# Optimization experiments

Measured on AMD Instinct MI355X. Metric: run time of the kernel, lower is better.

## Reference

```python
import jax, jax.numpy as jnp
import numpy as np
from jax import lax

LB, UB = 0.0, 0.1
N_ITERS = 32  # fixed-point iterations for water-filling rebalance


def _conv(x, w, b):
    y = lax.conv_general_dilated(x, w, (1, 1), ((1, 1), (1, 1)),
                                 dimension_numbers=("NCHW", "OIHW", "NCHW"))
    return y + b[None, :, None, None]


def _maxpool2(x):
    return lax.reduce_window(x, -jnp.inf, lax.max, (1, 1, 2, 2), (1, 1, 2, 2), "VALID")


def _linear(x, w, b):
    return x @ w.T + b


def _gru(x_num, W_ih, W_hh, b_ih, b_hh):
    # x_num: [B, S, N]; torch GRU gate order r, z, n
    B = x_num.shape[0]
    H = W_hh.shape[1]
    xs = jnp.swapaxes(x_num, 0, 1)  # [S, B, N]

    def step(h, x_t):
        gi = x_t @ W_ih.T + b_ih            # [B, 3H]
        gh = h @ W_hh.T + b_hh              # [B, 3H]
        i_r, i_z, i_n = jnp.split(gi, 3, axis=-1)
        h_r, h_z, h_n = jnp.split(gh, 3, axis=-1)
        r = jax.nn.sigmoid(i_r + h_r)
        z = jax.nn.sigmoid(i_z + h_z)
        n = jnp.tanh(i_n + r * h_n)
        h_new = (1.0 - z) * n + z * h
        return h_new, None

    h0 = jnp.zeros((B, H), dtype=x_num.dtype)
    h_last, _ = lax.scan(step, h0, xs)
    return h_last


def _rebalance_one(w):
    # vectorized fixed-point version of the per-sample while-loop water-filling
    def body(carry, _):
        old, wc = carry
        leftover = jnp.sum(old - wc)
        mask = wc != UB
        s = jnp.sum(jnp.where(mask, wc, 0.0))
        gift = jnp.where(mask & (s > 0), leftover * wc / jnp.where(s > 0, s, 1.0), 0.0)
        new_old = wc + gift
        new_wc = jnp.clip(new_old, LB, UB)
        return (new_old, new_wc), None

    init = (w, jnp.clip(w, LB, UB))
    (_, wc), _ = lax.scan(body, init, None, length=N_ITERS)
    return wc


def setup_inputs() -> dict:
    key = jax.random.key(0)
    ks = jax.random.split(key, 16)
    B, S, N, H_IMG, W_IMG, HID = 16, 60, 50, 64, 60, 128
    fc_in = 64 * (H_IMG // 4) * (W_IMG // 4)  # 15360
    sc = 0.05
    return {
        "x_num": jax.random.normal(ks[0], (B, S, N), jnp.float32),
        "x_img": jax.random.uniform(ks[1], (B, N, H_IMG, W_IMG), jnp.float32),
        "conv1_w": jax.random.normal(ks[2], (32, 1, 3, 3), jnp.float32) * sc,
        "conv1_b": jnp.zeros((32,), jnp.float32),
        "conv2_w": jax.random.normal(ks[3], (64, 32, 3, 3), jnp.float32) * sc,
        "conv2_b": jnp.zeros((64,), jnp.float32),
        "fc1_w": jax.random.normal(ks[4], (64, fc_in), jnp.float32) * 0.01,
        "fc1_b": jnp.zeros((64,), jnp.float32),
        "fc_binary_w": jax.random.normal(ks[5], (1, 64), jnp.float32) * sc,
        "fc_binary_b": jnp.zeros((1,), jnp.float32),
        "fc2_w": jax.random.normal(ks[6], (128, 64), jnp.float32) * sc,
        "fc2_b": jnp.zeros((128,), jnp.float32),
        "W_ih": jax.random.normal(ks[7], (3 * HID, N), jnp.float32) * sc,
        "W_hh": jax.random.normal(ks[8], (3 * HID, HID), jnp.float32) * sc,
        "b_ih": jnp.zeros((3 * HID,), jnp.float32),
        "b_hh": jnp.zeros((3 * HID,), jnp.float32),
        "gru_fc_w": jax.random.normal(ks[9], (N, HID), jnp.float32) * sc,
        "gru_fc_b": jnp.zeros((N,), jnp.float32),
        "fusion_w": jax.random.normal(ks[10], (64, N + 128), jnp.float32) * sc,
        "fusion_b": jnp.zeros((64,), jnp.float32),
        "final_w": jax.random.normal(ks[11], (N, 64), jnp.float32) * sc,
        "final_b": jnp.zeros((N,), jnp.float32),
    }


def reference(x_num, x_img, conv1_w, conv1_b, conv2_w, conv2_b, fc1_w, fc1_b,
              fc_binary_w, fc_binary_b, fc2_w, fc2_b, W_ih, W_hh, b_ih, b_hh,
              gru_fc_w, gru_fc_b, fusion_w, fusion_b, final_w, final_b):
    B, S, N = x_num.shape
    # GRU branch: last hidden -> Linear -> [B, N]
    h_last = _gru(x_num, W_ih, W_hh, b_ih, b_hh)
    numerical_features = _linear(h_last, gru_fc_w, gru_fc_b)

    # CNN branch on per-stock chart images
    xi = x_img.reshape(B * N, 1, x_img.shape[2], x_img.shape[3])
    h = _maxpool2(jax.nn.relu(_conv(xi, conv1_w, conv1_b)))
    h = _maxpool2(jax.nn.relu(_conv(h, conv2_w, conv2_b)))
    h = h.reshape(B * N, -1)
    feats = jax.nn.relu(_linear(h, fc1_w, fc1_b))
    binary_pred = jax.nn.sigmoid(_linear(feats, fc_binary_w, fc_binary_b))
    cnn_features = _linear(feats, fc2_w, fc2_b).reshape(B, N, -1).mean(axis=1)

    fused = jax.nn.relu(_linear(jnp.concatenate([numerical_features, cnn_features], axis=1), fusion_w, fusion_b))
    w = jax.nn.softmax(_linear(fused, final_w, final_b), axis=1)
    portfolio_weights = jax.vmap(_rebalance_one)(w)
    return portfolio_weights, binary_pred.reshape(B, N)
```

## Files before the change

kernel.cpp:

```cpp
#include <hip/hip_runtime.h>
#include <hip/hip_bf16.h>
#include <hip/hip_fp16.h>

typedef unsigned short ushort_t;
typedef short short8_t __attribute__((ext_vector_type(8)));
typedef _Float16 half8_t __attribute__((ext_vector_type(8)));
typedef _Float16 h2 __attribute__((ext_vector_type(2)));
typedef float f32x4 __attribute__((ext_vector_type(4)));
typedef float f32x16 __attribute__((ext_vector_type(16)));

#define NBATCH 16
#define SEQ    60
#define NSTK   50
#define HID    128
#define G3     384
#define NIMG   800
#define IH     64
#define IW     60
#define P1H    32
#define P1W    30
#define P2C    64
#define FCIN   15360

#define OFF_WHHF   0u
#define OFF_WPREP  24576u
#define OFF_WFC1   33792u
#define OFF_GI     525312u
#define OFF_HLAST  893952u
#define OFF_POOL2  896000u
#define OFF_FC2O   7040000u
#define OFF_PART   7142400u
#define OFF_W1H    7961600u
#define WS_FLOATS  7961760u

#define E_WHH  49152
#define E_WPR  18432
#define E_FC1  983040
#define E_W1H  160
#define E_TOT  (E_WHH + E_WPR + E_FC1 + E_W1H)

struct __align__(16) ConvS {
    ushort_t pool1t[18][4][32][8];
    union {
        float    imgp[35][60];
        ushort_t pool2s[64][120];
    } u;
};
struct __align__(16) GruS {
    ushort_t hb[2][16 * 136];
};
#define SMEM_BYTES 52224

__device__ __forceinline__ float fast_sig(float x) {
    const float e = __expf(-x);
    return __builtin_amdgcn_rcpf(1.f + e);
}
__device__ __forceinline__ float fast_tanh(float x) {
    const float xc = fmaxf(fminf(x, 15.f), -15.f);
    const float e = __expf(2.f * xc);
    return (e - 1.f) * __builtin_amdgcn_rcpf(e + 1.f);
}
__device__ __forceinline__ h2 hmax2v(h2 a, h2 b) {
    h2 r;
    r[0] = a[0] > b[0] ? a[0] : b[0];
    r[1] = a[1] > b[1] ? a[1] : b[1];
    return r;
}

__global__ __launch_bounds__(384) void k_pre(const float* __restrict__ xnum,
                                             const float* __restrict__ wih,
                                             const float* __restrict__ bih,
                                             const float* __restrict__ whh,
                                             const float* __restrict__ c2w,
                                             const float* __restrict__ fc1w,
                                             const float* __restrict__ c1w,
                                             const float* __restrict__ c1b,
                                             float* __restrict__ GI,
                                             ushort_t* __restrict__ whhf,
                                             ushort_t* __restrict__ wprep,
                                             ushort_t* __restrict__ wfc1,
                                             unsigned int* __restrict__ w1h)
{
    const int bid = blockIdx.x;
    if (bid < 960) {
        const int s = bid >> 4, b = bid & 15;
        const int j = threadIdx.x;
        const float* xr = xnum + (size_t)(b * SEQ + s) * NSTK;
        const float* wr = wih + (size_t)j * NSTK;
        float a = bih[j];
        #pragma unroll 10
        for (int k = 0; k < NSTK; ++k) a = fmaf(xr[k], wr[k], a);
        GI[((size_t)s * 16 + b) * G3 + j] = a;
        return;
    }
    const int idx = (bid - 960) * 384 + threadIdx.x;
    if (idx < E_WHH) {
        const int e = idx;
        const int i = e & 7, l = (e >> 3) & 63, ksj = e >> 9;
        const int ks = ksj & 3, jt = ksj >> 2;
        const int j = jt * 16 + (l & 15);
        const int k = ks * 32 + ((l >> 4) << 3) + i;
        __hip_bfloat16 hv = __float2bfloat16(whh[j * HID + k]);
        whhf[e] = *(ushort_t*)&hv;
    } else if (idx < E_WHH + E_WPR) {
        const int e = idx - E_WHH;
        const int i = e & 7, l = (e >> 3) & 63, rest = e >> 9;
        const int ks = rest & 1, mt = rest >> 1;
        const int tap = mt % 9, mm = mt / 9;
        const int oc = mm * 32 + (l & 31);
        const int ic = ks * 16 + ((l >> 5) << 3) + i;
        const _Float16 hv = (_Float16)c2w[((size_t)oc * 32 + ic) * 9 + tap];
        wprep[e] = *(const ushort_t*)&hv;
    } else if (idx < E_WHH + E_WPR + E_FC1) {
        const int e = idx - (E_WHH + E_WPR);
        const int i = e & 7, l = (e >> 3) & 63, rest = e >> 9;
        const int n = rest & 3, T = rest >> 2;
        const int oc = n * 16 + (l & 15);
        const int k = T * 32 + ((l >> 4) << 3) + i;
        __hip_bfloat16 hv = __float2bfloat16(fc1w[(size_t)oc * FCIN + k]);
        wfc1[e] = *(ushort_t*)&hv;
    } else if (idx < E_TOT) {
        const int e = idx - (E_WHH + E_WPR + E_FC1);
        if (e < 144) {
            const int p = e / 9, tap = e - p * 9;
            const int ch0 = (p >> 2) * 8 + (p & 3) * 2;
            const _Float16 lo = (_Float16)c1w[ch0 * 9 + tap];
            const _Float16 hi = (_Float16)c1w[(ch0 + 1) * 9 + tap];
            w1h[p * 9 + tap] = ((unsigned)*(const ushort_t*)&hi << 16) | *(const ushort_t*)&lo;
        } else {
            const int p = e - 144;
            const int ch0 = (p >> 2) * 8 + (p & 3) * 2;
            const _Float16 lo = (_Float16)c1b[ch0];
            const _Float16 hi = (_Float16)c1b[ch0 + 1];
            w1h[144 + p] = ((unsigned)*(const ushort_t*)&hi << 16) | *(const ushort_t*)&lo;
        }
    }
}

__global__ __launch_bounds__(512, 2) void k_mega(const float* __restrict__ x_img,
                                                 const unsigned int* __restrict__ w1h,
                                                 const float* __restrict__ c2b,
                                                 const ushort_t* __restrict__ wprep,
                                                 const float* __restrict__ GI,
                                                 const ushort_t* __restrict__ whhf,
                                                 const float* __restrict__ bhh,
                                                 ushort_t* __restrict__ pool2,
                                                 float* __restrict__ hlast)
{
    extern __shared__ char smraw[];
    const int tid = threadIdx.x;
    const int bid = blockIdx.x;

    if (bid == 0) {
        GruS* g = (GruS*)smraw;
        const int w = tid >> 6, l = tid & 63;
        const int arow = l & 15, kq = l >> 4;
        const int hh = w * 16 + (l & 15);
        const int b0 = (l >> 4) * 4;
        short8_t wfr[3][4];
        #pragma unroll
        for (int g3 = 0; g3 < 3; ++g3)
            #pragma unroll
            for (int ks = 0; ks < 4; ++ks)
                wfr[g3][ks] = *(const short8_t*)&whhf[((((g3 * 8 + w) * 4 + ks) * 64 + l) * 8)];
        const float bhr = bhh[hh];
        const float bhz = bhh[128 + hh];
        const float bhn = bhh[256 + hh];
        float h[4] = {0.f, 0.f, 0.f, 0.f};
        for (int i = tid; i < 1088; i += 512) ((unsigned int*)g->hb[0])[i] = 0u;
        __syncthreads();

        int cur = 0;
        for (int s = 0; s < SEQ; ++s) {
            const float* gis = GI + ((size_t)s * 16 + b0) * G3 + hh;
            float cr[4], cz[4], cn[4];
            #pragma unroll
            for (int r = 0; r < 4; ++r) {
                cr[r] = gis[r * G3];
                cz[r] = gis[r * G3 + 128];
                cn[r] = gis[r * G3 + 256];
            }
            f32x4 ar = {0.f, 0.f, 0.f, 0.f};
            f32x4 az = {0.f, 0.f, 0.f, 0.f};
            f32x4 an = {0.f, 0.f, 0.f, 0.f};
            #pragma unroll
            for (int ks = 0; ks < 4; ++ks) {
                const short8_t af = *(const short8_t*)&g->hb[cur][arow * 136 + ks * 32 + kq * 8];
                ar = __builtin_amdgcn_mfma_f32_16x16x32_bf16(af, wfr[0][ks], ar, 0, 0, 0);
                az = __builtin_amdgcn_mfma_f32_16x16x32_bf16(af, wfr[1][ks], az, 0, 0, 0);
                an = __builtin_amdgcn_mfma_f32_16x16x32_bf16(af, wfr[2][ks], an, 0, 0, 0);
            }
            const int nxt = cur ^ 1;
            #pragma unroll
            for (int r = 0; r < 4; ++r) {
                const float rg = fast_sig(cr[r] + ar[r] + bhr);
                const float zg = fast_sig(cz[r] + az[r] + bhz);
                const float ng = fast_tanh(cn[r] + rg * (an[r] + bhn));
                h[r] = (1.f - zg) * ng + zg * h[r];
                __hip_bfloat16 t = __float2bfloat16(h[r]);
                g->hb[nxt][(b0 + r) * 136 + hh] = *(ushort_t*)&t;
            }
            __syncthreads();
            cur = nxt;
        }
        #pragma unroll
        for (int r = 0; r < 4; ++r) hlast[(b0 + r) * HID + hh] = h[r];
        return;
    }

    ConvS* c = (ConvS*)smraw;
    const int img  = (bid - 1) >> 1;
    const int half = (bid - 1) & 1;
    const float* xim = x_img + (size_t)img * (IH * IW);
    const int rowbase = 29 * half;

    {
        const short8_t z = {0, 0, 0, 0, 0, 0, 0, 0};
        const int zrow = half ? 17 : 0;
        if (tid < 128) {
            const int cg = tid >> 5, xs = tid & 31;
            *(short8_t*)&c->pool1t[zrow][cg][xs][0] = z;
        } else if (tid < 272) {
            const int q = tid - 128;
            const int ly = q / 8, cg = (q >> 1) & 3, xs = (q & 1) * 31;
            *(short8_t*)&c->pool1t[ly][cg][xs][0] = z;
        }
    }
    {
        const f32x4* src = (const f32x4*)(xim + rowbase * IW);
        f32x4* dst = (f32x4*)c->u.imgp;
        for (int i = tid; i < 525; i += 512) dst[i] = src[i];
    }
    __syncthreads();

    if (tid < 510) {
        const int gj = tid / 30, px = tid - gj * 30;
        const int g = half * 15 + gj;
        const int ly = gj + 1 - half;
        const h2 z2 = {(_Float16)0.f, (_Float16)0.f};
        h2 patch2[4][4];
        #pragma unroll
        for (int yy = 0; yy < 4; ++yy) {
            const int giy = 2 * g - 1 + yy;
            const int liy = giy - rowbase;
            #pragma unroll
            for (int xx = 0; xx < 4; ++xx) {
                const int ix = 2 * px - 1 + xx;
                const float v = (giy >= 0 && giy < IH && ix >= 0 && ix < IW)
                                    ? c->u.imgp[liy][ix] : 0.f;
                const _Float16 vh = (_Float16)v;
                h2 p2; p2[0] = vh; p2[1] = vh;
                patch2[yy][xx] = p2;
            }
        }
        #pragma unroll
        for (int cg = 0; cg < 4; ++cg) {
            unsigned int ov[4];
            #pragma unroll
            for (int pr = 0; pr < 4; ++pr) {
                const int p = cg * 4 + pr;
                h2 wv[9];
                #pragma unroll
                for (int t = 0; t < 9; ++t) {
                    const unsigned int wu = w1h[p * 9 + t];
                    wv[t] = *(const h2*)&wu;
                }
                h2 a00 = z2, a01 = z2, a10 = z2, a11 = z2;
                #pragma unroll
                for (int ky = 0; ky < 3; ++ky)
                    #pragma unroll
                    for (int kx = 0; kx < 3; ++kx) {
                        const h2 wt = wv[ky * 3 + kx];
                        a00 = wt * patch2[ky][kx]     + a00;
                        a01 = wt * patch2[ky][kx + 1] + a01;
                        a10 = wt * patch2[ky + 1][kx] + a10;
                        a11 = wt * patch2[ky + 1][kx + 1] + a11;
                    }
                const unsigned int bu = w1h[144 + p];
                const h2 bia2 = *(const h2*)&bu;
                h2 m = hmax2v(hmax2v(a00, a01), hmax2v(a10, a11));
                h2 r = hmax2v(m + bia2, z2);
                ov[pr] = *(unsigned int*)&r;
            }
            *(uint4*)&c->pool1t[ly][cg][px + 1][0] = *(uint4*)ov;
        }
    }
    __syncthreads();

    {
        const int w  = tid >> 6, l = tid & 63;
        const int m  = w & 1;
        const int hi = l >> 5;
        const int col = l & 31;

        half8_t af[9][2];
        #pragma unroll
        for (int tap = 0; tap < 9; ++tap)
            #pragma unroll
            for (int ks = 0; ks < 2; ++ks)
                af[tap][ks] = *(const half8_t*)&wprep[(((m * 9 + tap) * 2 + ks) * 64 + l) * 8];
        float bia[16];
        #pragma unroll
        for (int r = 0; r < 16; ++r)
            bia[r] = c2b[m * 32 + (r & 3) + 8 * (r >> 2) + 4 * hi];

        const bool wr = ((col & 1) == 0) && (col < 30);
        const int px = col >> 1;

        #pragma unroll
        for (int yy = 0; yy < 2; ++yy) {
            const int ypl = (w >> 1) + yy * 4;
            f32x16 a0, a1;
            #pragma unroll
            for (int r = 0; r < 16; ++r) { a0[r] = 0.f; a1[r] = 0.f; }
            #pragma unroll
            for (int ro = 0; ro < 4; ++ro) {
                const int ly = 2 * ypl + ro;
                half8_t bf[3][2];
                #pragma unroll
                for (int kx = 0; kx < 3; ++kx)
                    #pragma unroll
                    for (int ks = 0; ks < 2; ++ks)
                        bf[kx][ks] = *(const half8_t*)&c->pool1t[ly][ks * 2 + hi][kx + col][0];
                if (ro < 3) {
                    #pragma unroll
                    for (int kx = 0; kx < 3; ++kx)
                        #pragma unroll
                        for (int ks = 0; ks < 2; ++ks)
                            a0 = __builtin_amdgcn_mfma_f32_32x32x16_f16(af[ro * 3 + kx][ks], bf[kx][ks], a0, 0, 0, 0);
                }
                if (ro >= 1) {
                    #pragma unroll
                    for (int kx = 0; kx < 3; ++kx)
                        #pragma unroll
                        for (int ks = 0; ks < 2; ++ks)
                            a1 = __builtin_amdgcn_mfma_f32_32x32x16_f16(af[(ro - 1) * 3 + kx][ks], bf[kx][ks], a1, 0, 0, 0);
                }
            }
            #pragma unroll
            for (int r = 0; r < 16; ++r) {
                float v = fmaxf(a0[r], a1[r]);
                v = fmaxf(v, __shfl_xor(v, 1, 64));
                v = fmaxf(v + bia[r], 0.f);
                if (wr) {
                    const int oc = m * 32 + (r & 3) + 8 * (r >> 2) + 4 * hi;
                    __hip_bfloat16 hv = __float2bfloat16(v);
                    c->u.pool2s[oc][ypl * 15 + px] = *(ushort_t*)&hv;
                }
            }
        }
        __syncthreads();
        {
            int4* dst = (int4*)(pool2 + (size_t)img * FCIN);
            const int4* src = (const int4*)c->u.pool2s;
            #pragma unroll
            for (int jj = 0; jj < 2; ++jj) {
                const int i = tid + jj * 512;
                if (i < 960) {
                    const int oc = i / 15, cc = i - oc * 15;
                    dst[oc * 30 + half * 15 + cc] = src[i];
                }
            }
        }
    }
}

__global__ __launch_bounds__(256) void k_fc1(const ushort_t* __restrict__ pool2,
                                             const ushort_t* __restrict__ wfc1,
                                             float* __restrict__ part)
{
    const int mt = blockIdx.x >> 4;
    const int ks = blockIdx.x & 15;
    const int n = threadIdx.x >> 6, l = threadIdx.x & 63;
    const int arow = l & 15, kq = l >> 4;
    const int img16 = mt * 16;
    const ushort_t* Ab = pool2 + (size_t)(img16 + arow) * FCIN + ks * 960 + kq * 8;
    const ushort_t* Bb = wfc1 + ((size_t)(ks * 30 * 4 + n) * 64 + l) * 8;
    f32x4 acc0 = {0.f, 0.f, 0.f, 0.f}, acc1 = {0.f, 0.f, 0.f, 0.f};
    #pragma unroll 10
    for (int t = 0; t < 30; t += 2) {
        const short8_t aA = *(const short8_t*)(Ab + (size_t)t * 32);
        const short8_t bA = *(const short8_t*)(Bb + (size_t)t * 2048);
        const short8_t aB = *(const short8_t*)(Ab + (size_t)(t + 1) * 32);
        const short8_t bB = *(const short8_t*)(Bb + (size_t)(t + 1) * 2048);
        acc0 = __builtin_amdgcn_mfma_f32_16x16x32_bf16(aA, bA, acc0, 0, 0, 0);
        acc1 = __builtin_amdgcn_mfma_f32_16x16x32_bf16(aB, bB, acc1, 0, 0, 0);
    }
    float* dst = &part[((size_t)ks * NIMG + img16 + kq * 4) * 64 + n * 16 + arow];
    #pragma unroll
    for (int r = 0; r < 4; ++r)
        dst[(size_t)r * 64] = acc0[r] + acc1[r];
}

__device__ __forceinline__ float wave_sum(float v) {
    #pragma unroll
    for (int o = 32; o > 0; o >>= 1) v += __shfl_xor(v, o, 64);
    return v;
}
__device__ __forceinline__ float wave_max(float v) {
    #pragma unroll
    for (int o = 32; o > 0; o >>= 1) v = fmaxf(v, __shfl_xor(v, o, 64));
    return v;
}

__global__ __launch_bounds__(512) void k_post(const float* __restrict__ part,
                                              const float* __restrict__ fc1b,
                                              const float* __restrict__ fbw,
                                              const float* __restrict__ fbb,
                                              const float* __restrict__ fc2w,
                                              const float* __restrict__ fc2b,
                                              float* __restrict__ out,
                                              float* __restrict__ fc2o)
{
    const int t = threadIdx.x;
    const int im8 = t >> 6;
    const int tl = t & 63;
    const int img = blockIdx.x * 8 + im8;
    float s = fc1b[tl];
    #pragma unroll
    for (int ks = 0; ks < 16; ++ks) s += part[((size_t)ks * NIMG + img) * 64 + tl];
    const float f = fmaxf(s, 0.f);
    __shared__ float flc[8][64];
    flc[im8][tl] = f;
    const float bs = wave_sum(f * fbw[tl]);
    if (tl == 0) out[800 + img] = 1.f / (1.f + expf(-(bs + fbb[0])));
    __syncthreads();
    #pragma unroll
    for (int q = 0; q < 2; ++q) {
        const int j = tl + q * 64;
        float a2 = fc2b[j];
        #pragma unroll 8
        for (int k = 0; k < 64; ++k) a2 = fmaf(flc[im8][k], fc2w[j * 64 + k], a2);
        fc2o[(size_t)img * 128 + j] = a2;
    }
}

__global__ __launch_bounds__(64) void k_final(const float* __restrict__ hlast,
                                              const float* __restrict__ fc2o,
                                              const float* __restrict__ gw,
                                              const float* __restrict__ gb,
                                              const float* __restrict__ fw,
                                              const float* __restrict__ fb,
                                              const float* __restrict__ finw,
                                              const float* __restrict__ finb,
                                              float* __restrict__ out)
{
    const int b = blockIdx.x, t = threadIdx.x;
    __shared__ float cf[128], nf[64], fu[64];
    #pragma unroll
    for (int jj = 0; jj < 2; ++jj) {
        const int j = t + jj * 64;
        float s = 0.f;
        for (int n = 0; n < NSTK; ++n) s += fc2o[(size_t)(b * NSTK + n) * 128 + j];
        cf[j] = s * (1.0f / 50.0f);
    }
    float s = 0.f;
    if (t < NSTK) {
        s = gb[t];
        for (int k = 0; k < HID; ++k) s = fmaf(hlast[b * HID + k], gw[t * HID + k], s);
    }
    nf[t] = (t < NSTK) ? s : 0.f;
    __syncthreads();
    float f = fb[t];
    for (int k = 0; k < NSTK; ++k) f = fmaf(nf[k], fw[t * 178 + k], f);
    for (int k = 0; k < 128; ++k) f = fmaf(cf[k], fw[t * 178 + 50 + k], f);
    fu[t] = fmaxf(f, 0.f);
    __syncthreads();
    float L = -3.4e38f;
    if (t < NSTK) {
        L = finb[t];
        for (int k = 0; k < 64; ++k) L = fmaf(fu[k], finw[t * 64 + k], L);
    }
    const float m = wave_max(L);
    const float e = (t < NSTK) ? expf(L - m) : 0.f;
    const float se = wave_sum(e);
    const float wv = e / se;
    float old = wv;
    float wc = fminf(fmaxf(wv, 0.f), 0.1f);
    for (int it = 0; it < 32; ++it) {
        const float leftover = wave_sum(old - wc);
        const bool mask = (wc != 0.1f);
        const float ssum = wave_sum(mask ? wc : 0.f);
        const float gift = (mask && ssum > 0.f) ? leftover * wc / ssum : 0.f;
        old = wc + gift;
        wc = fminf(fmaxf(old, 0.f), 0.1f);
    }
    if (t < NSTK) out[b * NSTK + t] = wc;
}

extern "C" void kernel_launch(void* const* d_in, const int* in_sizes, int n_in,
                              void* d_out, int out_size, void* d_ws, size_t ws_size,
                              hipStream_t stream)
{
    const float* x_num = (const float*)d_in[0];
    const float* x_img = (const float*)d_in[1];
    const float* c1w  = (const float*)d_in[2];
    const float* c1b  = (const float*)d_in[3];
    const float* c2w  = (const float*)d_in[4];
    const float* c2b  = (const float*)d_in[5];
    const float* fc1w = (const float*)d_in[6];
    const float* fc1b = (const float*)d_in[7];
    const float* fbw  = (const float*)d_in[8];
    const float* fbb  = (const float*)d_in[9];
    const float* fc2w = (const float*)d_in[10];
    const float* fc2b = (const float*)d_in[11];
    const float* wih  = (const float*)d_in[12];
    const float* whh  = (const float*)d_in[13];
    const float* bih  = (const float*)d_in[14];
    const float* bhh  = (const float*)d_in[15];
    const float* gw   = (const float*)d_in[16];
    const float* gb   = (const float*)d_in[17];
    const float* fw   = (const float*)d_in[18];
    const float* fb   = (const float*)d_in[19];
    const float* finw = (const float*)d_in[20];
    const float* finb = (const float*)d_in[21];
    float* out = (float*)d_out;
    float* ws  = (float*)d_ws;
    if (ws_size < (size_t)WS_FLOATS * 4) return;

    ushort_t* whhf  = (ushort_t*)(ws + OFF_WHHF);
    ushort_t* wprep = (ushort_t*)(ws + OFF_WPREP);
    ushort_t* wfc1  = (ushort_t*)(ws + OFF_WFC1);
    float* GI       = ws + OFF_GI;
    float* hlast    = ws + OFF_HLAST;
    ushort_t* pool2 = (ushort_t*)(ws + OFF_POOL2);
    float* fc2o     = ws + OFF_FC2O;
    float* part     = ws + OFF_PART;
    unsigned int* w1h = (unsigned int*)(ws + OFF_W1H);

    (void)hipFuncSetAttribute(reinterpret_cast<const void*>(k_mega),
                              hipFuncAttributeMaxDynamicSharedMemorySize, SMEM_BYTES);

    k_pre   <<<960 + 2737, 384, 0, stream>>>(x_num, wih, bih, whh, c2w, fc1w, c1w, c1b,
                                             GI, whhf, wprep, wfc1, w1h);
    k_mega  <<<2 * NIMG + 1, 512, SMEM_BYTES, stream>>>(x_img, w1h, c2b, wprep,
                                                        GI, whhf, bhh, pool2, hlast);
    k_fc1   <<<50 * 16, 256, 0, stream>>>(pool2, wfc1, part);
    k_post  <<<100, 512, 0, stream>>>(part, fc1b, fbw, fbb, fc2w, fc2b, out, fc2o);
    k_final <<<NBATCH, 64, 0, stream>>>(hlast, fc2o, gw, gb, fw, fb, finw, finb, out);
}
```

Before: 138.4 us.

## Move GRU recurrence from CNN mega-kernel into post-processing kernel

Splits the GRU recurrence block out of the combined CNN kernel and runs it as an extra block in the post-fc1 kernel. The CNN kernel becomes homogeneous, dropping the block-0 branch and its shared-memory and register needs. In exchange, the serial GRU loop no longer overlaps with the convolution work and may become exposed on the critical path after fc1.

```diff
diff --git a/kernel.cpp b/kernel.cpp
--- a/kernel.cpp
+++ b/kernel.cpp
@@ -137,80 +137,19 @@
     }
 }
 
-__global__ __launch_bounds__(512, 2) void k_mega(const float* __restrict__ x_img,
-                                                 const unsigned int* __restrict__ w1h,
-                                                 const float* __restrict__ c2b,
-                                                 const ushort_t* __restrict__ wprep,
-                                                 const float* __restrict__ GI,
-                                                 const ushort_t* __restrict__ whhf,
-                                                 const float* __restrict__ bhh,
-                                                 ushort_t* __restrict__ pool2,
-                                                 float* __restrict__ hlast)
+__global__ __launch_bounds__(512, 2) void k_cnn(const float* __restrict__ x_img,
+                                                const unsigned int* __restrict__ w1h,
+                                                const float* __restrict__ c2b,
+                                                const ushort_t* __restrict__ wprep,
+                                                ushort_t* __restrict__ pool2)
 {
     extern __shared__ char smraw[];
     const int tid = threadIdx.x;
     const int bid = blockIdx.x;
 
-    if (bid == 0) {
-        GruS* g = (GruS*)smraw;
-        const int w = tid >> 6, l = tid & 63;
-        const int arow = l & 15, kq = l >> 4;
-        const int hh = w * 16 + (l & 15);
-        const int b0 = (l >> 4) * 4;
-        short8_t wfr[3][4];
-        #pragma unroll
-        for (int g3 = 0; g3 < 3; ++g3)
-            #pragma unroll
-            for (int ks = 0; ks < 4; ++ks)
-                wfr[g3][ks] = *(const short8_t*)&whhf[((((g3 * 8 + w) * 4 + ks) * 64 + l) * 8)];
-        const float bhr = bhh[hh];
-        const float bhz = bhh[128 + hh];
-        const float bhn = bhh[256 + hh];
-        float h[4] = {0.f, 0.f, 0.f, 0.f};
-        for (int i = tid; i < 1088; i += 512) ((unsigned int*)g->hb[0])[i] = 0u;
-        __syncthreads();
-
-        int cur = 0;
-        for (int s = 0; s < SEQ; ++s) {
-            const float* gis = GI + ((size_t)s * 16 + b0) * G3 + hh;
-            float cr[4], cz[4], cn[4];
-            #pragma unroll
-            for (int r = 0; r < 4; ++r) {
-                cr[r] = gis[r * G3];
-                cz[r] = gis[r * G3 + 128];
-                cn[r] = gis[r * G3 + 256];
-            }
-            f32x4 ar = {0.f, 0.f, 0.f, 0.f};
-            f32x4 az = {0.f, 0.f, 0.f, 0.f};
-            f32x4 an = {0.f, 0.f, 0.f, 0.f};
-            #pragma unroll
-            for (int ks = 0; ks < 4; ++ks) {
-                const short8_t af = *(const short8_t*)&g->hb[cur][arow * 136 + ks * 32 + kq * 8];
-                ar = __builtin_amdgcn_mfma_f32_16x16x32_bf16(af, wfr[0][ks], ar, 0, 0, 0);
-                az = __builtin_amdgcn_mfma_f32_16x16x32_bf16(af, wfr[1][ks], az, 0, 0, 0);
-                an = __builtin_amdgcn_mfma_f32_16x16x32_bf16(af, wfr[2][ks], an, 0, 0, 0);
-            }
-            const int nxt = cur ^ 1;
-            #pragma unroll
-            for (int r = 0; r < 4; ++r) {
-                const float rg = fast_sig(cr[r] + ar[r] + bhr);
-                const float zg = fast_sig(cz[r] + az[r] + bhz);
-                const float ng = fast_tanh(cn[r] + rg * (an[r] + bhn));
-                h[r] = (1.f - zg) * ng + zg * h[r];
-                __hip_bfloat16 t = __float2bfloat16(h[r]);
-                g->hb[nxt][(b0 + r) * 136 + hh] = *(ushort_t*)&t;
-            }
-            __syncthreads();
-            cur = nxt;
-        }
-        #pragma unroll
-        for (int r = 0; r < 4; ++r) hlast[(b0 + r) * HID + hh] = h[r];
-        return;
-    }
-
     ConvS* c = (ConvS*)smraw;
-    const int img  = (bid - 1) >> 1;
-    const int half = (bid - 1) & 1;
+    const int img  = bid >> 1;
+    const int half = bid & 1;
     const float* xim = x_img + (size_t)img * (IH * IW);
     const int rowbase = 29 * half;
 
@@ -403,24 +342,87 @@
     return v;
 }
 
-__global__ __launch_bounds__(512) void k_post(const float* __restrict__ part,
-                                              const float* __restrict__ fc1b,
-                                              const float* __restrict__ fbw,
-                                              const float* __restrict__ fbb,
-                                              const float* __restrict__ fc2w,
-                                              const float* __restrict__ fc2b,
-                                              float* __restrict__ out,
-                                              float* __restrict__ fc2o)
+__global__ __launch_bounds__(512, 2) void k_postgru(const float* __restrict__ part,
+                                                    const float* __restrict__ fc1b,
+                                                    const float* __restrict__ fbw,
+                                                    const float* __restrict__ fbb,
+                                                    const float* __restrict__ fc2w,
+                                                    const float* __restrict__ fc2b,
+                                                    const float* __restrict__ GI,
+                                                    const ushort_t* __restrict__ whhf,
+                                                    const float* __restrict__ bhh,
+                                                    float* __restrict__ out,
+                                                    float* __restrict__ fc2o,
+                                                    float* __restrict__ hlast)
 {
-    const int t = threadIdx.x;
-    const int im8 = t >> 6;
-    const int tl = t & 63;
+    __shared__ __align__(16) char sm[8704];
+    const int tid = threadIdx.x;
+
+    if (blockIdx.x == 100) {
+        GruS* g = (GruS*)sm;
+        const int w = tid >> 6, l = tid & 63;
+        const int arow = l & 15, kq = l >> 4;
+        const int hh = w * 16 + (l & 15);
+        const int b0 = (l >> 4) * 4;
+        short8_t wfr[3][4];
+        #pragma unroll
+        for (int g3 = 0; g3 < 3; ++g3)
+            #pragma unroll
+            for (int ks = 0; ks < 4; ++ks)
+                wfr[g3][ks] = *(const short8_t*)&whhf[((((g3 * 8 + w) * 4 + ks) * 64 + l) * 8)];
+        const float bhr = bhh[hh];
+        const float bhz = bhh[128 + hh];
+        const float bhn = bhh[256 + hh];
+        float h[4] = {0.f, 0.f, 0.f, 0.f};
+        for (int i = tid; i < 1088; i += 512) ((unsigned int*)g->hb[0])[i] = 0u;
+        __syncthreads();
+
+        int cur = 0;
+        for (int s = 0; s < SEQ; ++s) {
+            const float* gis = GI + ((size_t)s * 16 + b0) * G3 + hh;
+            float cr[4], cz[4], cn[4];
+            #pragma unroll
+            for (int r = 0; r < 4; ++r) {
+                cr[r] = gis[r * G3];
+                cz[r] = gis[r * G3 + 128];
+                cn[r] = gis[r * G3 + 256];
+            }
+            f32x4 ar = {0.f, 0.f, 0.f, 0.f};
+            f32x4 az = {0.f, 0.f, 0.f, 0.f};
+            f32x4 an = {0.f, 0.f, 0.f, 0.f};
+            #pragma unroll
+            for (int ks = 0; ks < 4; ++ks) {
+                const short8_t af = *(const short8_t*)&g->hb[cur][arow * 136 + ks * 32 + kq * 8];
+                ar = __builtin_amdgcn_mfma_f32_16x16x32_bf16(af, wfr[0][ks], ar, 0, 0, 0);
+                az = __builtin_amdgcn_mfma_f32_16x16x32_bf16(af, wfr[1][ks], az, 0, 0, 0);
+                an = __builtin_amdgcn_mfma_f32_16x16x32_bf16(af, wfr[2][ks], an, 0, 0, 0);
+            }
+            const int nxt = cur ^ 1;
+            #pragma unroll
+            for (int r = 0; r < 4; ++r) {
+                const float rg = fast_sig(cr[r] + ar[r] + bhr);
+                const float zg = fast_sig(cz[r] + az[r] + bhz);
+                const float ng = fast_tanh(cn[r] + rg * (an[r] + bhn));
+                h[r] = (1.f - zg) * ng + zg * h[r];
+                __hip_bfloat16 t = __float2bfloat16(h[r]);
+                g->hb[nxt][(b0 + r) * 136 + hh] = *(ushort_t*)&t;
+            }
+            __syncthreads();
+            cur = nxt;
+        }
+        #pragma unroll
+        for (int r = 0; r < 4; ++r) hlast[(b0 + r) * HID + hh] = h[r];
+        return;
+    }
+
+    float (*flc)[64] = (float(*)[64])sm;
+    const int im8 = tid >> 6;
+    const int tl = tid & 63;
     const int img = blockIdx.x * 8 + im8;
     float s = fc1b[tl];
     #pragma unroll
     for (int ks = 0; ks < 16; ++ks) s += part[((size_t)ks * NIMG + img) * 64 + tl];
     const float f = fmaxf(s, 0.f);
-    __shared__ float flc[8][64];
     flc[im8][tl] = f;
     const float bs = wave_sum(f * fbw[tl]);
     if (tl == 0) out[800 + img] = 1.f / (1.f + expf(-(bs + fbb[0])));
@@ -528,14 +530,14 @@
     float* part     = ws + OFF_PART;
     unsigned int* w1h = (unsigned int*)(ws + OFF_W1H);
 
-    (void)hipFuncSetAttribute(reinterpret_cast<const void*>(k_mega),
+    (void)hipFuncSetAttribute(reinterpret_cast<const void*>(k_cnn),
                               hipFuncAttributeMaxDynamicSharedMemorySize, SMEM_BYTES);
 
-    k_pre   <<<960 + 2737, 384, 0, stream>>>(x_num, wih, bih, whh, c2w, fc1w, c1w, c1b,
-                                             GI, whhf, wprep, wfc1, w1h);
-    k_mega  <<<2 * NIMG + 1, 512, SMEM_BYTES, stream>>>(x_img, w1h, c2b, wprep,
-                                                        GI, whhf, bhh, pool2, hlast);
-    k_fc1   <<<50 * 16, 256, 0, stream>>>(pool2, wfc1, part);
-    k_post  <<<100, 512, 0, stream>>>(part, fc1b, fbw, fbb, fc2w, fc2b, out, fc2o);
-    k_final <<<NBATCH, 64, 0, stream>>>(hlast, fc2o, gw, gb, fw, fb, finw, finb, out);
-}
+    k_pre     <<<960 + 2737, 384, 0, stream>>>(x_num, wih, bih, whh, c2w, fc1w, c1w, c1b,
+                                               GI, whhf, wprep, wfc1, w1h);
+    k_cnn     <<<2 * NIMG, 512, SMEM_BYTES, stream>>>(x_img, w1h, c2b, wprep, pool2);
+    k_fc1     <<<50 * 16, 256, 0, stream>>>(pool2, wfc1, part);
+    k_postgru <<<101, 512, 0, stream>>>(part, fc1b, fbw, fbb, fc2w, fc2b,
+                                        GI, whhf, bhh, out, fc2o, hlast);
+    k_final   <<<NBATCH, 64, 0, stream>>>(hlast, fc2o, gw, gb, fw, fb, finw, finb, out);
+}
```

New measurement: 189.6 us. +37.0%, slower.
